# Performance work log

Measured on AMD Instinct MI355X. Metric: run time of the kernel, lower is better.

Reference implementation:

```python
import jax, jax.numpy as jnp
import numpy as np

T, B, INP, HID, OUT = 512, 256, 128, 256, 64
DT = 0.1   # self.dt
CPL = 0.1  # coupling_strength

def _lin(v, W, b):
    # nn.Linear: v @ W.T + b, W has shape (out, in)
    return v @ W.T + b

def setup_inputs() -> dict:
    key = jax.random.key(0)
    ks = jax.random.split(key, 20)
    def W(k, o, i, gain=0.5):
        return (jax.random.normal(k, (o, i), jnp.float32) * gain / np.sqrt(i)).astype(jnp.float32)
    z = lambda n: jnp.zeros((n,), jnp.float32)
    return {
        "x": jax.random.normal(ks[0], (T, B, INP), jnp.float32),
        "W_h_w": W(ks[1], HID, HID), "W_h_b": z(HID),
        "U_h_w": W(ks[2], HID, INP), "U_h_b": z(HID),
        "W_tau_h_w": W(ks[3], HID, HID, 0.1), "W_tau_h_b": z(HID),
        "b_h": z(HID),
        "W_z_real_w": W(ks[4], HID, HID), "W_z_real_b": z(HID),
        "W_z_imag_w": W(ks[5], HID, HID), "W_z_imag_b": z(HID),
        "U_z_w": W(ks[6], HID, INP), "U_z_b": z(HID),
        "W_tau_z_w": W(ks[7], HID, HID, 0.1), "W_tau_z_b": z(HID),
        "b_z_real": z(HID), "b_z_imag": z(HID),
        "h2z_w": W(ks[8], HID, HID, 1.0), "h2z_b": jax.random.normal(ks[9], (HID,), jnp.float32) * 0.01,
        "z2h_w": W(ks[10], HID, HID, 1.0), "z2h_b": jax.random.normal(ks[11], (HID,), jnp.float32) * 0.01,
        "out_h_w": W(ks[12], OUT, HID, 1.0), "out_h_b": jax.random.normal(ks[13], (OUT,), jnp.float32) * 0.01,
        "out_z_w": W(ks[14], OUT, HID, 1.0), "out_z_b": jax.random.normal(ks[15], (OUT,), jnp.float32) * 0.01,
    }

def reference(x, W_h_w, W_h_b, U_h_w, U_h_b, W_tau_h_w, W_tau_h_b, b_h,
              W_z_real_w, W_z_real_b, W_z_imag_w, W_z_imag_b, U_z_w, U_z_b,
              W_tau_z_w, W_tau_z_b, b_z_real, b_z_imag,
              h2z_w, h2z_b, z2h_w, z2h_b, out_h_w, out_h_b, out_z_w, out_z_b):
    # Complex state z is carried as (zr, zi) real pair; math is identical to
    # torch.complex handling (coupling uses z.real, tau_z uses |z|).
    def step(carry, x_t):
        h, zr, zi = carry
        # dh/dt (uses old h, old z -- matches torch loop ordering)
        tau_h = jnp.clip(jax.nn.sigmoid(_lin(h, W_tau_h_w, W_tau_h_b)), 0.01, 1.0) + 1e-6
        dh = (-h + jnp.tanh(_lin(h, W_h_w, W_h_b)) + _lin(x_t, U_h_w, U_h_b)
              + b_h + CPL * _lin(zr, z2h_w, z2h_b)) / tau_h
        # dz/dt (uses old h, old z)
        zabs = jnp.sqrt(zr * zr + zi * zi + 1e-24)  # |z|, eps for grad safety at 0
        tau_z = jnp.clip(jax.nn.sigmoid(_lin(zabs, W_tau_z_w, W_tau_z_b)), 0.01, 1.0) + 1e-6
        uzx = _lin(x_t, U_z_w, U_z_b)
        ch = CPL * _lin(h, h2z_w, h2z_b)
        dzr = (-zr + jnp.tanh(_lin(zr, W_z_real_w, W_z_real_b)) + uzx + b_z_real + ch) / tau_z
        dzi = (-zi + jnp.tanh(_lin(zi, W_z_imag_w, W_z_imag_b)) + uzx + b_z_imag + ch) / tau_z
        h_n = h + DT * dh
        zr_n = zr + DT * dzr
        zi_n = zi + DT * dzi
        y = _lin(h_n, out_h_w, out_h_b) + _lin(zr_n, out_z_w, out_z_b)
        return (h_n, zr_n, zi_n), y
    z0 = jnp.zeros((B, HID), x.dtype)
    _, y = jax.lax.scan(step, (z0, z0, z0), x)
    return y  # (T, B, OUT)
```

## Files before the change

### kernel.cpp

```cpp
#include <hip/hip_runtime.h>
#include <hip/hip_bf16.h>
#include <math.h>

#define T_    512
#define B_    256
#define INP_  128
#define HID_  256
#define OUT_  64
#define DT_   0.1f
#define CPL_  0.1f

typedef __attribute__((ext_vector_type(8))) short          bf16x8;
typedef __attribute__((ext_vector_type(4))) float          f32x4;
typedef __attribute__((ext_vector_type(4))) unsigned short u16x4;

#define G_WH    0
#define G_WTAUH 1
#define G_WZR   2
#define G_WZI   3
#define G_WTAUZ 4
#define G_H2Z   5
#define G_Z2H   6
#define UH     458752
#define UZ     491520
#define OH     524288
#define OZ     540672
#define NW_TOTAL 557056
#define BIAS_OFF_BYTES (NW_TOTAL * 2)
#define BT_H    0
#define BTAU_H  256
#define BH_TOT  512
#define BT_ZR   768
#define BT_ZI   1024
#define BTAU_Z  1280
#define BZR_TOT 1536
#define BZI_TOT 1792
#define BY      2048
#define REGION_OFF_BYTES (BIAS_OFF_BYTES + 8448)
#define POISON32 0x7FC07FC0u
#define POISON64 0x7FC07FC07FC07FC0ull

__device__ __forceinline__ unsigned short f2bf(float f) {
    unsigned int u = __float_as_uint(f);
    u += 0x7fffu + ((u >> 16) & 1u);
    return (unsigned short)(u >> 16);
}

__device__ __forceinline__ float rcp_(float x) { return __builtin_amdgcn_rcpf(x); }
__device__ __forceinline__ float sigmoid_fast(float x) {
    return rcp_(1.0f + __expf(-x));
}
__device__ __forceinline__ float tanh_fast(float x) {
    return 1.0f - 2.0f * rcp_(__expf(2.0f * x) + 1.0f);
}

#define AGLD(p) __hip_atomic_load((p), __ATOMIC_RELAXED, __HIP_MEMORY_SCOPE_AGENT)
#define AGST(p, v) __hip_atomic_store((p), (v), __ATOMIC_RELAXED, __HIP_MEMORY_SCOPE_AGENT)

__global__ void prep_weights(const float* __restrict__ Wh,   const float* __restrict__ Wtauh,
                             const float* __restrict__ Wzr,  const float* __restrict__ Wzi,
                             const float* __restrict__ Wtauz,const float* __restrict__ h2z,
                             const float* __restrict__ z2h,  const float* __restrict__ Uh,
                             const float* __restrict__ Uz,   const float* __restrict__ oh,
                             const float* __restrict__ oz,   unsigned short* __restrict__ ws) {
    int fid = blockIdx.x * 256 + threadIdx.x;
    if (fid >= NW_TOTAL / 8) return;
    int o = fid * 8;
    const float* src;
    int row, col, K;
    float scale = 1.0f;
    if (o < UH) {
        int g  = o >> 16;
        int r  = o & 65535;
        int T  = r >> 12;
        int r2 = r & 4095;
        int kt = r2 >> 9;
        int l  = (r2 & 511) >> 3;
        row = T * 16 + (l & 15);
        col = kt * 32 + (l >> 4) * 8;
        K = 256;
        if      (g == G_WH)    src = Wh;
        else if (g == G_WTAUH) src = Wtauh;
        else if (g == G_WZR)   src = Wzr;
        else if (g == G_WZI)   src = Wzi;
        else if (g == G_WTAUZ) src = Wtauz;
        else if (g == G_H2Z)   { src = h2z; scale = CPL_; }
        else                   { src = z2h; scale = CPL_; }
    } else if (o < OH) {
        int g  = (o - UH) >> 15;
        int r  = (o - UH) & 32767;
        int T  = r >> 11;
        int r2 = r & 2047;
        int kt = r2 >> 9;
        int l  = (r2 & 511) >> 3;
        row = T * 16 + (l & 15);
        col = kt * 32 + (l >> 4) * 8;
        K = 128;
        src = g ? Uz : Uh;
    } else {
        int g  = (o - OH) >> 14;
        int r  = (o - OH) & 16383;
        int T  = r >> 12;
        int r2 = r & 4095;
        int kt = r2 >> 9;
        int l  = (r2 & 511) >> 3;
        row = T * 16 + (l & 15);
        col = kt * 32 + (l >> 4) * 8;
        K = 256;
        src = g ? oz : oh;
    }
    const float* p = src + (size_t)row * K + col;
    float4 v0 = *(const float4*)p;
    float4 v1 = *(const float4*)(p + 4);
    u16x4 a, b;
    a.x = f2bf(v0.x * scale); a.y = f2bf(v0.y * scale);
    a.z = f2bf(v0.z * scale); a.w = f2bf(v0.w * scale);
    b.x = f2bf(v1.x * scale); b.y = f2bf(v1.y * scale);
    b.z = f2bf(v1.z * scale); b.w = f2bf(v1.w * scale);
    *(u16x4*)(ws + o)     = a;
    *(u16x4*)(ws + o + 4) = b;
}

__global__ void prep_bias(const float* __restrict__ Whb,  const float* __restrict__ Wtauhb,
                          const float* __restrict__ Uhb,  const float* __restrict__ bh,
                          const float* __restrict__ z2hb, const float* __restrict__ Wzrb,
                          const float* __restrict__ Wzib, const float* __restrict__ Wtauzb,
                          const float* __restrict__ Uzb,  const float* __restrict__ bzr,
                          const float* __restrict__ bzi,  const float* __restrict__ h2zb,
                          const float* __restrict__ ohb,  const float* __restrict__ ozb,
                          float* __restrict__ bias) {
    int n = threadIdx.x;
    if (n < 256) {
        bias[BT_H + n]    = Whb[n];
        bias[BTAU_H + n]  = Wtauhb[n];
        bias[BH_TOT + n]  = Uhb[n] + bh[n] + CPL_ * z2hb[n];
        bias[BT_ZR + n]   = Wzrb[n];
        bias[BT_ZI + n]   = Wzib[n];
        bias[BTAU_Z + n]  = Wtauzb[n];
        bias[BZR_TOT + n] = Uzb[n] + bzr[n] + CPL_ * h2zb[n];
        bias[BZI_TOT + n] = Uzb[n] + bzi[n] + CPL_ * h2zb[n];
        if (n < 64) bias[BY + n] = ohb[n] + ozb[n];
    }
}

__global__ void prep_poison(unsigned long long* __restrict__ p) {
    const size_t nslot0 = 16ull * 4096;
    const size_t ntot   = 513ull * 16 * 4096;
    for (size_t i = (size_t)blockIdx.x * 512 + threadIdx.x; i < ntot;
         i += (size_t)gridDim.x * 512)
        p[i] = (i < nslot0) ? 0ull : POISON64;
}

__global__ void prep_zero(unsigned long long* __restrict__ p) {
    int i = blockIdx.x * 512 + threadIdx.x;
    if (i < 135168) p[i] = 0;
}

template<int NKT>
__device__ __forceinline__ void wload(bf16x8* w, const unsigned short* __restrict__ p, int loff) {
#pragma unroll
    for (int kt = 0; kt < NKT; ++kt) w[kt] = *(const bf16x8*)(p + kt * 512 + loff);
}

template<int NKT>
__device__ __forceinline__ void wgemm(const bf16x8* a, const bf16x8* w, f32x4& acc) {
#pragma unroll
    for (int kt = 0; kt < NKT; ++kt)
        acc = __builtin_amdgcn_mfma_f32_16x16x32_bf16(a[kt], w[kt], acc, 0, 0, 0);
}

__device__ __forceinline__ bf16x8 loadXfrag(const float* __restrict__ xrow, int off) {
    float4 v0 = *(const float4*)(xrow + off);
    float4 v1 = *(const float4*)(xrow + off + 4);
    bf16x8 r;
    r[0] = (short)f2bf(v0.x); r[1] = (short)f2bf(v0.y);
    r[2] = (short)f2bf(v0.z); r[3] = (short)f2bf(v0.w);
    r[4] = (short)f2bf(v1.x); r[5] = (short)f2bf(v1.y);
    r[6] = (short)f2bf(v1.z); r[7] = (short)f2bf(v1.w);
    return r;
}

__device__ __forceinline__ void loadAimg(const char* st, int m16, int hi, bf16x8* a) {
    const unsigned long long* b = (const unsigned long long*)
        (st + ((hi >> 1) * 512 + m16 * 32 + (hi & 1) * 16));
#pragma unroll
    for (int kt = 0; kt < 8; ++kt) {
        union { unsigned long long q[2]; bf16x8 v; } u;
        u.q[0] = AGLD(b + kt * 128);
        u.q[1] = AGLD(b + kt * 128 + 1);
        a[kt] = u.v;
    }
}

__device__ __forceinline__ int chkq(unsigned long long q) {
    return ((unsigned)q == POISON32) || ((unsigned)(q >> 32) == POISON32);
}

__device__ __forceinline__ void pollA2(const char* slot, int m16, int hi,
                                       bf16x8* a0, bf16x8* a1) {
    const size_t off = (size_t)((hi >> 1) * 512 + m16 * 32 + (hi & 1) * 16);
    const unsigned long long* b0 = (const unsigned long long*)(slot + off);
    const unsigned long long* b1 = (const unsigned long long*)(slot + 8192 + off);
    unsigned long long q0[16], q1[16];
    for (;;) {
        int dirty = 0;
#pragma unroll
        for (int kt = 0; kt < 8; ++kt) {
            q0[2 * kt]     = AGLD(b0 + kt * 128);
            q0[2 * kt + 1] = AGLD(b0 + kt * 128 + 1);
            q1[2 * kt]     = AGLD(b1 + kt * 128);
            q1[2 * kt + 1] = AGLD(b1 + kt * 128 + 1);
        }
#pragma unroll
        for (int i = 0; i < 16; ++i) dirty |= chkq(q0[i]) | chkq(q1[i]);
        if (!__any(dirty)) break;
        __builtin_amdgcn_s_sleep(1);
    }
#pragma unroll
    for (int kt = 0; kt < 8; ++kt) {
        union { unsigned long long q[2]; bf16x8 v; } u;
        u.q[0] = q0[2 * kt]; u.q[1] = q0[2 * kt + 1]; a0[kt] = u.v;
        u.q[0] = q1[2 * kt]; u.q[1] = q1[2 * kt + 1]; a1[kt] = u.v;
    }
}

__device__ __forceinline__ void pollA4(const char* slot, int m16, int hi,
                                       bf16x8* a0, bf16x8* a1, bf16x8* a2, bf16x8* a3) {
    const size_t off = (size_t)((hi >> 1) * 512 + m16 * 32 + (hi & 1) * 16);
    const unsigned long long* b0 = (const unsigned long long*)(slot + off);
    const unsigned long long* b1 = (const unsigned long long*)(slot + 8192 + off);
    const unsigned long long* b2 = (const unsigned long long*)(slot + 16384 + off);
    const unsigned long long* b3 = (const unsigned long long*)(slot + 24576 + off);
    unsigned long long q0[16], q1[16], q2[16], q3[16];
    for (;;) {
        int dirty = 0;
#pragma unroll
        for (int kt = 0; kt < 8; ++kt) {
            q0[2 * kt]     = AGLD(b0 + kt * 128);
            q0[2 * kt + 1] = AGLD(b0 + kt * 128 + 1);
            q1[2 * kt]     = AGLD(b1 + kt * 128);
            q1[2 * kt + 1] = AGLD(b1 + kt * 128 + 1);
            q2[2 * kt]     = AGLD(b2 + kt * 128);
            q2[2 * kt + 1] = AGLD(b2 + kt * 128 + 1);
            q3[2 * kt]     = AGLD(b3 + kt * 128);
            q3[2 * kt + 1] = AGLD(b3 + kt * 128 + 1);
        }
#pragma unroll
        for (int i = 0; i < 16; ++i)
            dirty |= chkq(q0[i]) | chkq(q1[i]) | chkq(q2[i]) | chkq(q3[i]);
        if (!__any(dirty)) break;
        __builtin_amdgcn_s_sleep(1);
    }
#pragma unroll
    for (int kt = 0; kt < 8; ++kt) {
        union { unsigned long long q[2]; bf16x8 v; } u;
        u.q[0] = q0[2 * kt]; u.q[1] = q0[2 * kt + 1]; a0[kt] = u.v;
        u.q[0] = q1[2 * kt]; u.q[1] = q1[2 * kt + 1]; a1[kt] = u.v;
        u.q[0] = q2[2 * kt]; u.q[1] = q2[2 * kt + 1]; a2[kt] = u.v;
        u.q[0] = q3[2 * kt]; u.q[1] = q3[2 * kt + 1]; a3[kt] = u.v;
    }
}

__device__ __forceinline__ void pub_rm(char* gslot, int m16, int hi, const float* v) {
    const int odd = m16 & 1;
    float oth[4];
#pragma unroll
    for (int j = 0; j < 4; ++j) oth[j] = __shfl_xor(v[j], 1);
#pragma unroll
    for (int k = 0; k < 2; ++k) {
        const int j = odd * 2 + k;
        const int r = hi * 4 + j;
        unsigned a = f2bf(v[j]), b = f2bf(oth[j]);
        unsigned u = odd ? (b | (a << 16)) : (a | (b << 16));
        AGST((unsigned*)(gslot + r * 32 + (m16 & ~1) * 2), u);
    }
}

__launch_bounds__(256, 1)
__global__ void twistor_poll(const float* __restrict__ x, unsigned short* __restrict__ ws,
                             float* __restrict__ y) {
    const int tid  = threadIdx.x;
    const int lane = tid & 63;
    const int w    = tid >> 6;
    const int half = w >> 1;
    const int role = w & 1;
    const int m16  = lane & 15;
    const int hi   = lane >> 4;
    const int loff = lane * 8;
    const int bid  = blockIdx.x;
    const int rg   = bid & 15;
    const int cg   = bid >> 4;
    const int tt   = cg * 2 + half;
    const int brow0 = rg * 16;
    const int n    = tt * 16 + m16;
    const float* bias = (const float*)((const char*)ws + BIAS_OFF_BYTES);
    char* simg = (char*)ws + REGION_OFF_BYTES;

    bf16x8 wA[8], wB[8], wC[8], wU[4];
    bf16x8 wO[8], wO2[8];
    bf16x8 wTZ[8];
    if (role == 0) {
        wload<8>(wA, ws + G_WH    * 65536 + tt * 4096, loff);
        wload<8>(wB, ws + G_WTAUH * 65536 + tt * 4096, loff);
        wload<8>(wC, ws + G_Z2H   * 65536 + tt * 4096, loff);
        wload<4>(wU, ws + UH + tt * 2048, loff);
        if (tt < 4) {
            wload<8>(wO,  ws + OH + tt * 4096, loff);
            wload<8>(wO2, ws + OZ + tt * 4096, loff);
        }
    } else {
        wload<8>(wA, ws + G_WZR   * 65536 + tt * 4096, loff);
        wload<8>(wB, ws + G_WZI   * 65536 + tt * 4096, loff);
        wload<8>(wC, ws + G_H2Z   * 65536 + tt * 4096, loff);
        wload<4>(wU, ws + UZ + tt * 2048, loff);
        wload<8>(wTZ, ws + G_WTAUZ * 65536 + tt * 4096, loff);
    }

    const float bthh = bias[BT_H + n],    btauh = bias[BTAU_H + n], bht = bias[BH_TOT + n];
    const float btzr = bias[BT_ZR + n],   btzi  = bias[BT_ZI + n],  btauz = bias[BTAU_Z + n];
    const float bzrt = bias[BZR_TOT + n], bzit  = bias[BZI_TOT + n];
    const float by_  = (tt < 4 && role == 0) ? bias[BY + n] : 0.f;

    float s0_[4] = {0, 0, 0, 0};
    float s1_[4] = {0, 0, 0, 0};

    for (int t = 0; t < T_; ++t) {
        bf16x8 ax[4];
        {
            const float* xrow = x + ((size_t)t * B_ + brow0 + m16) * INP_;
#pragma unroll
            for (int kt = 0; kt < 4; ++kt) ax[kt] = loadXfrag(xrow, kt * 32 + hi * 8);
        }
        const char* slotR = simg + ((size_t)t * 16 + rg) * 32768;
        char*       slotW = simg + ((size_t)(t + 1) * 16 + rg) * 32768;

        if (role == 0) {
            bf16x8 ah[8], azr[8];
            pollA2(slotR, m16, hi, ah, azr);
            const bool ydo = (tt < 4) && (t > 0);
            f32x4 a_y = {0.f, 0.f, 0.f, 0.f};
            if (ydo) { wgemm<8>(ah, wO, a_y); wgemm<8>(azr, wO2, a_y); }
            f32x4 a_th = {0.f, 0.f, 0.f, 0.f}, a_tau = {0.f, 0.f, 0.f, 0.f};
            f32x4 a_ch = {0.f, 0.f, 0.f, 0.f};
            wgemm<8>(ah,  wA, a_th);
            wgemm<8>(ah,  wB, a_tau);
            wgemm<8>(azr, wC, a_ch);
            wgemm<4>(ax,  wU, a_ch);
            if (ydo) {
#pragma unroll
                for (int j = 0; j < 4; ++j)
                    y[((size_t)(t - 1) * B_ + brow0 + hi * 4 + j) * OUT_ + n] =
                        a_y[j] + by_;
            }
            float hn[4];
#pragma unroll
            for (int j = 0; j < 4; ++j) {
                float th = fminf(fmaxf(sigmoid_fast(a_tau[j] + btauh), 0.01f), 1.0f) + 1e-6f;
                float dh = -s0_[j] + tanh_fast(a_th[j] + bthh) + a_ch[j] + bht;
                hn[j]    = s0_[j] + DT_ * dh * rcp_(th);
                s0_[j] = hn[j];
            }
            pub_rm(slotW + tt * 512, m16, hi, hn);
        } else {
            bf16x8 ah[8], azr[8], azi[8], aza[8];
            pollA4(slotR, m16, hi, ah, azr, azi, aza);
            f32x4 a_tzr = {0.f, 0.f, 0.f, 0.f}, a_tzi = {0.f, 0.f, 0.f, 0.f};
            f32x4 a_tz  = {0.f, 0.f, 0.f, 0.f}, a_cz  = {0.f, 0.f, 0.f, 0.f};
            wgemm<8>(azr, wA,  a_tzr);
            wgemm<8>(ah,  wC,  a_cz);
            wgemm<8>(azi, wB,  a_tzi);
            wgemm<8>(aza, wTZ, a_tz);
            wgemm<4>(ax,  wU,  a_cz);
            float zrn[4], zin[4], zan[4];
#pragma unroll
            for (int j = 0; j < 4; ++j) {
                float tz  = fminf(fmaxf(sigmoid_fast(a_tz[j] + btauz), 0.01f), 1.0f) + 1e-6f;
                float rtz = rcp_(tz);
                float dzr = -s0_[j] + tanh_fast(a_tzr[j] + btzr) + a_cz[j] + bzrt;
                float dzi = -s1_[j] + tanh_fast(a_tzi[j] + btzi) + a_cz[j] + bzit;
                zrn[j] = s0_[j] + DT_ * dzr * rtz;
                zin[j] = s1_[j] + DT_ * dzi * rtz;
                zan[j] = sqrtf(zrn[j] * zrn[j] + zin[j] * zin[j] + 1e-24f);
                s0_[j] = zrn[j]; s1_[j] = zin[j];
            }
            pub_rm(slotW + 8192  + tt * 512, m16, hi, zrn);
            pub_rm(slotW + 16384 + tt * 512, m16, hi, zin);
            pub_rm(slotW + 24576 + tt * 512, m16, hi, zan);
        }
    }

    if (role == 0 && tt < 4) {
        const char* slotR = simg + ((size_t)T_ * 16 + rg) * 32768;
        bf16x8 ah[8], azr[8];
        pollA2(slotR, m16, hi, ah, azr);
        f32x4 a_y = {0.f, 0.f, 0.f, 0.f};
        wgemm<8>(ah,  wO,  a_y);
        wgemm<8>(azr, wO2, a_y);
#pragma unroll
        for (int j = 0; j < 4; ++j)
            y[((size_t)(T_ - 1) * B_ + brow0 + hi * 4 + j) * OUT_ + n] = a_y[j] + by_;
    }
}

__device__ __forceinline__ void waitflags(const unsigned* flg, int lane, unsigned tgt) {
    for (;;) {
        unsigned v = tgt;
        if (lane < 32) v = AGLD(flg + lane * 16);
        if (__all((int)(v >= tgt))) break;
        __builtin_amdgcn_s_sleep(1);
    }
}
__device__ __forceinline__ void postflag(unsigned* myflag, int lane, unsigned val) {
    asm volatile("s_waitcnt vmcnt(0)" ::: "memory");
    if (lane == 0) AGST(myflag, val);
}

__launch_bounds__(256, 1)
__global__ void twistor_flag(const float* __restrict__ x, unsigned short* __restrict__ ws,
                             float* __restrict__ y) {
    const int tid  = threadIdx.x;
    const int lane = tid & 63;
    const int w    = tid >> 6;
    const int half = w >> 1;
    const int role = w & 1;
    const int m16  = lane & 15;
    const int hi   = lane >> 4;
    const int loff = lane * 8;
    const int bid  = blockIdx.x;
    const int rg   = bid & 15;
    const int cg   = bid >> 4;
    const int tt   = cg * 2 + half;
    const int brow0 = rg * 16;
    const int n    = tt * 16 + m16;
    const float* bias = (const float*)((const char*)ws + BIAS_OFF_BYTES);
    unsigned* flg    = (unsigned*)((char*)ws + REGION_OFF_BYTES) + rg * 512;
    unsigned* myflag = flg + (tt * 2 + role) * 16;
    char* simg = (char*)ws + REGION_OFF_BYTES + 32768;

    bf16x8 wA[8], wB[8], wC[8], wU[4];
    bf16x8 wO[8], wO2[8];
    bf16x8 wTZ[8];
    if (role == 0) {
        wload<8>(wA, ws + G_WH    * 65536 + tt * 4096, loff);
        wload<8>(wB, ws + G_WTAUH * 65536 + tt * 4096, loff);
        wload<8>(wC, ws + G_Z2H   * 65536 + tt * 4096, loff);
        wload<4>(wU, ws + UH + tt * 2048, loff);
        if (tt < 4) {
            wload<8>(wO,  ws + OH + tt * 4096, loff);
            wload<8>(wO2, ws + OZ + tt * 4096, loff);
        }
    } else {
        wload<8>(wA, ws + G_WZR   * 65536 + tt * 4096, loff);
        wload<8>(wB, ws + G_WZI   * 65536 + tt * 4096, loff);
        wload<8>(wC, ws + G_H2Z   * 65536 + tt * 4096, loff);
        wload<4>(wU, ws + UZ + tt * 2048, loff);
        wload<8>(wTZ, ws + G_WTAUZ * 65536 + tt * 4096, loff);
    }

    const float bthh = bias[BT_H + n],    btauh = bias[BTAU_H + n], bht = bias[BH_TOT + n];
    const float btzr = bias[BT_ZR + n],   btzi  = bias[BT_ZI + n],  btauz = bias[BTAU_Z + n];
    const float bzrt = bias[BZR_TOT + n], bzit  = bias[BZI_TOT + n];
    const float by_  = (tt < 4 && role == 0) ? bias[BY + n] : 0.f;

    float s0_[4] = {0, 0, 0, 0};
    float s1_[4] = {0, 0, 0, 0};

    for (int t = 0; t < T_; ++t) {
        bf16x8 ax[4];
        {
            const float* xrow = x + ((size_t)t * B_ + brow0 + m16) * INP_;
#pragma unroll
            for (int kt = 0; kt < 4; ++kt) ax[kt] = loadXfrag(xrow, kt * 32 + hi * 8);
        }
        if (t > 0) waitflags(flg, lane, (unsigned)t);

        const char* imgR = simg + (size_t)((t & 1) * 16 + rg) * 32768;
        char*       imgW = simg + (size_t)(((t + 1) & 1) * 16 + rg) * 32768;

        bf16x8 ah[8], azr[8];
        loadAimg(imgR,        m16, hi, ah);
        loadAimg(imgR + 8192, m16, hi, azr);

        if (role == 0) {
            const bool ydo = (tt < 4) && (t > 0);
            f32x4 a_y = {0.f, 0.f, 0.f, 0.f};
            if (ydo) { wgemm<8>(ah, wO, a_y); wgemm<8>(azr, wO2, a_y); }
            f32x4 a_th = {0.f, 0.f, 0.f, 0.f}, a_tau = {0.f, 0.f, 0.f, 0.f};
            f32x4 a_ch = {0.f, 0.f, 0.f, 0.f};
            wgemm<8>(ah,  wA, a_th);
            wgemm<8>(ah,  wB, a_tau);
            wgemm<8>(azr, wC, a_ch);
            wgemm<4>(ax,  wU, a_ch);
            if (ydo) {
#pragma unroll
                for (int j = 0; j < 4; ++j)
                    y[((size_t)(t - 1) * B_ + brow0 + hi * 4 + j) * OUT_ + n] =
                        a_y[j] + by_;
            }
            float hn[4];
#pragma unroll
            for (int j = 0; j < 4; ++j) {
                float th = fminf(fmaxf(sigmoid_fast(a_tau[j] + btauh), 0.01f), 1.0f) + 1e-6f;
                float dh = -s0_[j] + tanh_fast(a_th[j] + bthh) + a_ch[j] + bht;
                hn[j]    = s0_[j] + DT_ * dh * rcp_(th);
                s0_[j] = hn[j];
            }
            pub_rm(imgW + tt * 512, m16, hi, hn);
        } else {
            bf16x8 azi[8], aza[8];
            loadAimg(imgR + 16384, m16, hi, azi);
            loadAimg(imgR + 24576, m16, hi, aza);
            f32x4 a_tzr = {0.f, 0.f, 0.f, 0.f}, a_tzi = {0.f, 0.f, 0.f, 0.f};
            f32x4 a_tz  = {0.f, 0.f, 0.f, 0.f}, a_cz  = {0.f, 0.f, 0.f, 0.f};
            wgemm<8>(azr, wA,  a_tzr);
            wgemm<8>(ah,  wC,  a_cz);
            wgemm<8>(azi, wB,  a_tzi);
            wgemm<8>(aza, wTZ, a_tz);
            wgemm<4>(ax,  wU,  a_cz);
            float zrn[4], zin[4], zan[4];
#pragma unroll
            for (int j = 0; j < 4; ++j) {
                float tz  = fminf(fmaxf(sigmoid_fast(a_tz[j] + btauz), 0.01f), 1.0f) + 1e-6f;
                float rtz = rcp_(tz);
                float dzr = -s0_[j] + tanh_fast(a_tzr[j] + btzr) + a_cz[j] + bzrt;
                float dzi = -s1_[j] + tanh_fast(a_tzi[j] + btzi) + a_cz[j] + bzit;
                zrn[j] = s0_[j] + DT_ * dzr * rtz;
                zin[j] = s1_[j] + DT_ * dzi * rtz;
                zan[j] = sqrtf(zrn[j] * zrn[j] + zin[j] * zin[j] + 1e-24f);
                s0_[j] = zrn[j]; s1_[j] = zin[j];
            }
            pub_rm(imgW + 8192  + tt * 512, m16, hi, zrn);
            pub_rm(imgW + 16384 + tt * 512, m16, hi, zin);
            pub_rm(imgW + 24576 + tt * 512, m16, hi, zan);
        }
        postflag(myflag, lane, (unsigned)(t + 1));
    }

    if (role == 0 && tt < 4) {
        waitflags(flg, lane, (unsigned)T_);
        const char* imgR = simg + (size_t)((T_ & 1) * 16 + rg) * 32768;
        bf16x8 ah[8], azr[8];
        loadAimg(imgR,        m16, hi, ah);
        loadAimg(imgR + 8192, m16, hi, azr);
        f32x4 a_y = {0.f, 0.f, 0.f, 0.f};
        wgemm<8>(ah,  wO,  a_y);
        wgemm<8>(azr, wO2, a_y);
#pragma unroll
        for (int j = 0; j < 4; ++j)
            y[((size_t)(T_ - 1) * B_ + brow0 + hi * 4 + j) * OUT_ + n] = a_y[j] + by_;
    }
}

extern "C" void kernel_launch(void* const* d_in, const int* in_sizes, int n_in,
                              void* d_out, int out_size, void* d_ws, size_t ws_size,
                              hipStream_t stream) {
    const float* x = (const float*)d_in[0];
    unsigned short* ws = (unsigned short*)d_ws;
    float* bias = (float*)((char*)d_ws + BIAS_OFF_BYTES);

    prep_weights<<<(NW_TOTAL / 8 + 255) / 256, 256, 0, stream>>>(
        (const float*)d_in[1],
        (const float*)d_in[5],
        (const float*)d_in[8],
        (const float*)d_in[10],
        (const float*)d_in[14],
        (const float*)d_in[18],
        (const float*)d_in[20],
        (const float*)d_in[3],
        (const float*)d_in[12],
        (const float*)d_in[22],
        (const float*)d_in[24],
        ws);
    prep_bias<<<1, 256, 0, stream>>>(
        (const float*)d_in[2],
        (const float*)d_in[6],
        (const float*)d_in[4],
        (const float*)d_in[7],
        (const float*)d_in[21],
        (const float*)d_in[9],
        (const float*)d_in[11],
        (const float*)d_in[15],
        (const float*)d_in[13],
        (const float*)d_in[16],
        (const float*)d_in[17],
        (const float*)d_in[19],
        (const float*)d_in[23],
        (const float*)d_in[25],
        bias);

    const size_t pollNeed = (size_t)REGION_OFF_BYTES + 513ull * 16 * 32768;
    if (ws_size >= pollNeed) {
        prep_poison<<<8192, 512, 0, stream>>>(
            (unsigned long long*)((char*)d_ws + REGION_OFF_BYTES));
        twistor_poll<<<128, 256, 0, stream>>>(x, ws, (float*)d_out);
    } else {
        prep_zero<<<264, 512, 0, stream>>>(
            (unsigned long long*)((char*)d_ws + REGION_OFF_BYTES));
        twistor_flag<<<128, 256, 0, stream>>>(x, ws, (float*)d_out);
    }
}
```

Before: 2.657 ms.

## Replace per-timestep exchange slots with a 4-deep poisoned ring buffer

The cross-block state exchange used one 32 KB slot group per timestep (513 groups), which had to be pre-poisoned by a large prep kernel and left every write in fresh memory. It now uses a 4-entry ring that is reused modulo 4. Each block re-poisons slot t+2 after reading slot t, and waits on vmcnt before publishing so the poison lands first. This shrinks the prep pass and the working set so the exchange can stay in cache. The cost is extra poison stores and a store drain each step, and correctness now depends on blocks never drifting more than two steps apart.

Measured after the change: 3.038 ms. 1.14x slower.

```diff
diff --git a/kernel.cpp b/kernel.cpp
--- a/kernel.cpp
+++ b/kernel.cpp
@@ -143,12 +143,9 @@
     }
 }
 
-__global__ void prep_poison(unsigned long long* __restrict__ p) {
-    const size_t nslot0 = 16ull * 4096;
-    const size_t ntot   = 513ull * 16 * 4096;
-    for (size_t i = (size_t)blockIdx.x * 512 + threadIdx.x; i < ntot;
-         i += (size_t)gridDim.x * 512)
-        p[i] = (i < nslot0) ? 0ull : POISON64;
+__global__ void prep_ring(unsigned long long* __restrict__ p) {
+    size_t i = (size_t)blockIdx.x * 512 + threadIdx.x;
+    if (i < 262144) p[i] = (i < 65536) ? 0ull : POISON64;
 }
 
 __global__ void prep_zero(unsigned long long* __restrict__ p) {
@@ -276,8 +273,17 @@
     }
 }
 
+__device__ __forceinline__ void pub_poison(char* gslot, int m16, int hi) {
+    const int odd = m16 & 1;
+#pragma unroll
+    for (int k = 0; k < 2; ++k) {
+        const int r = hi * 4 + odd * 2 + k;
+        AGST((unsigned*)(gslot + r * 32 + (m16 & ~1) * 2), POISON32);
+    }
+}
+
 __launch_bounds__(256, 1)
-__global__ void twistor_poll(const float* __restrict__ x, unsigned short* __restrict__ ws,
+__global__ void twistor_ring(const float* __restrict__ x, unsigned short* __restrict__ ws,
                              float* __restrict__ y) {
     const int tid  = threadIdx.x;
     const int lane = tid & 63;
@@ -331,12 +337,14 @@
 #pragma unroll
             for (int kt = 0; kt < 4; ++kt) ax[kt] = loadXfrag(xrow, kt * 32 + hi * 8);
         }
-        const char* slotR = simg + ((size_t)t * 16 + rg) * 32768;
-        char*       slotW = simg + ((size_t)(t + 1) * 16 + rg) * 32768;
+        const char* slotR = simg + ((size_t)(t & 3) * 16 + rg) * 32768;
+        char*       slotW = simg + ((size_t)((t + 1) & 3) * 16 + rg) * 32768;
+        char*       slotP = simg + ((size_t)((t + 2) & 3) * 16 + rg) * 32768;
 
         if (role == 0) {
             bf16x8 ah[8], azr[8];
             pollA2(slotR, m16, hi, ah, azr);
+            pub_poison(slotP + tt * 512, m16, hi);
             const bool ydo = (tt < 4) && (t > 0);
             f32x4 a_y = {0.f, 0.f, 0.f, 0.f};
             if (ydo) { wgemm<8>(ah, wO, a_y); wgemm<8>(azr, wO2, a_y); }
@@ -360,10 +368,14 @@
                 hn[j]    = s0_[j] + DT_ * dh * rcp_(th);
                 s0_[j] = hn[j];
             }
+            asm volatile("s_waitcnt vmcnt(0)" ::: "memory");
             pub_rm(slotW + tt * 512, m16, hi, hn);
         } else {
             bf16x8 ah[8], azr[8], azi[8], aza[8];
             pollA4(slotR, m16, hi, ah, azr, azi, aza);
+            pub_poison(slotP + 8192  + tt * 512, m16, hi);
+            pub_poison(slotP + 16384 + tt * 512, m16, hi);
+            pub_poison(slotP + 24576 + tt * 512, m16, hi);
             f32x4 a_tzr = {0.f, 0.f, 0.f, 0.f}, a_tzi = {0.f, 0.f, 0.f, 0.f};
             f32x4 a_tz  = {0.f, 0.f, 0.f, 0.f}, a_cz  = {0.f, 0.f, 0.f, 0.f};
             wgemm<8>(azr, wA,  a_tzr);
@@ -383,6 +395,7 @@
                 zan[j] = sqrtf(zrn[j] * zrn[j] + zin[j] * zin[j] + 1e-24f);
                 s0_[j] = zrn[j]; s1_[j] = zin[j];
             }
+            asm volatile("s_waitcnt vmcnt(0)" ::: "memory");
             pub_rm(slotW + 8192  + tt * 512, m16, hi, zrn);
             pub_rm(slotW + 16384 + tt * 512, m16, hi, zin);
             pub_rm(slotW + 24576 + tt * 512, m16, hi, zan);
@@ -390,7 +403,7 @@
     }
 
     if (role == 0 && tt < 4) {
-        const char* slotR = simg + ((size_t)T_ * 16 + rg) * 32768;
+        const char* slotR = simg + ((size_t)(T_ & 3) * 16 + rg) * 32768;
         bf16x8 ah[8], azr[8];
         pollA2(slotR, m16, hi, ah, azr);
         f32x4 a_y = {0.f, 0.f, 0.f, 0.f};
@@ -588,11 +601,11 @@
         (const float*)d_in[25],
         bias);
 
-    const size_t pollNeed = (size_t)REGION_OFF_BYTES + 513ull * 16 * 32768;
-    if (ws_size >= pollNeed) {
-        prep_poison<<<8192, 512, 0, stream>>>(
+    const size_t ringNeed = (size_t)REGION_OFF_BYTES + 4ull * 16 * 32768;
+    if (ws_size >= ringNeed) {
+        prep_ring<<<512, 512, 0, stream>>>(
             (unsigned long long*)((char*)d_ws + REGION_OFF_BYTES));
-        twistor_poll<<<128, 256, 0, stream>>>(x, ws, (float*)d_out);
+        twistor_ring<<<128, 256, 0, stream>>>(x, ws, (float*)d_out);
     } else {
         prep_zero<<<264, 512, 0, stream>>>(
             (unsigned long long*)((char*)d_ws + REGION_OFF_BYTES));
```
